# Optimization experiments

Measured on AMD Instinct MI355X. Metric: run time of the kernel, lower is better.

## Reference

```python
import jax, jax.numpy as jnp
import numpy as np

B, N, D, S, H, ITERS = 8, 2048, 256, 8, 256, 3
EPS = 1e-8
LN_EPS = 1e-5
SCALE = D ** -0.5


def _ln(x):
    # normalize over last axis (affine applied separately per slot)
    mu = jnp.mean(x, axis=-1, keepdims=True)
    var = jnp.var(x, axis=-1, keepdims=True)
    return (x - mu) / jnp.sqrt(var + LN_EPS)


def setup_inputs() -> dict:
    key = jax.random.key(0)
    ks = jax.random.split(key, 24)
    w = lambda k, shape, fan_in: jax.random.normal(k, shape, jnp.float32) / np.sqrt(fan_in)
    inp = {
        "inputs": jax.random.normal(ks[0], (B, N, D), jnp.float32),
        "slot_noise": jax.random.normal(ks[1], (B, S, D), jnp.float32),
        "slots_mu": jax.random.normal(ks[2], (1, S, D), jnp.float32),
        "slots_logsigma": 0.01 * jax.random.normal(ks[3], (1, S, D), jnp.float32),
        # per-slot LayerNorm affines [S, D]
        "g_in": jnp.ones((S, D), jnp.float32), "b_in": jnp.zeros((S, D), jnp.float32),
        "g_ns": jnp.ones((S, D), jnp.float32), "b_ns": jnp.zeros((S, D), jnp.float32),
        "g_pf": jnp.ones((S, D), jnp.float32), "b_pf": jnp.zeros((S, D), jnp.float32),
        # per-slot Linear weights [S, out, in] (torch convention)
        "Wq": w(ks[4], (S, D, D), D), "bq": jnp.zeros((S, D), jnp.float32),
        "Wk": w(ks[5], (S, D, D), D), "bk": jnp.zeros((S, D), jnp.float32),
        "Wv": w(ks[6], (S, D, D), D), "bv": jnp.zeros((S, D), jnp.float32),
        # per-slot GRUCell: [S, 3D, D] (gates order r, z, n as in torch)
        "W_ih": w(ks[7], (S, 3 * D, D), D), "b_ih": jnp.zeros((S, 3 * D), jnp.float32),
        "W_hh": w(ks[8], (S, 3 * D, D), D), "b_hh": jnp.zeros((S, 3 * D), jnp.float32),
        # per-slot MLP (dim -> hidden -> dim)
        "W1": w(ks[9], (S, H, D), D), "b1": jnp.zeros((S, H), jnp.float32),
        "W2": w(ks[10], (S, D, H), H), "b2": jnp.zeros((S, D), jnp.float32),
    }
    return inp


def slot_attention_fwd(inputs, slot_noise, slots_mu, slots_logsigma,
                       g_in, b_in, g_ns, b_ns, g_pf, b_pf,
                       Wq, bq, Wk, bk, Wv, bv,
                       W_ih, b_ih, W_hh, b_hh,
                       W1, b1, W2, b2):
    # slots init: mu + sigma * noise  -> [B, S, D]
    slots = slots_mu + jnp.exp(slots_logsigma) * slot_noise

    # per-slot LayerNorm of inputs: normalization is slot-independent, affine is per-slot
    xn = _ln(inputs)  # [B, N, D]
    inputs_n = xn[:, None, :, :] * g_in[None, :, None, :] + b_in[None, :, None, :]  # [B,S,N,D]

    # per-slot k/v projections as one batched GEMM over the slot axis
    k = jnp.einsum('bsnd,sod->bsno', inputs_n, Wk) + bk[None, :, None, :]  # [B,S,N,D]
    v = jnp.einsum('bsnd,sod->bsno', inputs_n, Wv) + bv[None, :, None, :]

    attn_ori = None
    for _ in range(ITERS):
        slots_prev = slots
        sn = _ln(slots) * g_ns[None] + b_ns[None]                     # [B,S,D]
        q = jnp.einsum('bsd,sod->bso', sn, Wq) + bq[None]             # [B,S,D]
        dots = jnp.einsum('bsd,bsnd->bsn', q, k) * SCALE              # [B,S,N]
        attn_ori = jax.nn.softmax(dots, axis=1) + EPS                 # softmax over slots
        attn = attn_ori / jnp.sum(attn_ori, axis=-1, keepdims=True)   # renormalize over n
        updates = jnp.einsum('bsnd,bsn->bsd', v, attn)                # [B,S,D]

        # per-slot GRUCell: h' = (1-z)*n + z*h
        gi = jnp.einsum('bsd,sod->bso', updates, W_ih) + b_ih[None]   # [B,S,3D]
        gh = jnp.einsum('bsd,sod->bso', slots_prev, W_hh) + b_hh[None]
        gi_r, gi_z, gi_n = jnp.split(gi, 3, axis=-1)
        gh_r, gh_z, gh_n = jnp.split(gh, 3, axis=-1)
        r = jax.nn.sigmoid(gi_r + gh_r)
        z = jax.nn.sigmoid(gi_z + gh_z)
        nn_ = jnp.tanh(gi_n + r * gh_n)
        slots = (1.0 - z) * nn_ + z * slots_prev

        # per-slot MLP residual
        pre = _ln(slots) * g_pf[None] + b_pf[None]
        h1 = jax.nn.relu(jnp.einsum('bsd,shd->bsh', pre, W1) + b1[None])
        slots = slots + jnp.einsum('bsh,sdh->bsd', h1, W2) + b2[None]

    return slots, attn_ori


def reference(inputs, slot_noise, slots_mu, slots_logsigma,
              g_in, b_in, g_ns, b_ns, g_pf, b_pf,
              Wq, bq, Wk, bk, Wv, bv,
              W_ih, b_ih, W_hh, b_hh,
              W1, b1, W2, b2):
    return slot_attention_fwd(inputs, slot_noise, slots_mu, slots_logsigma,
                              g_in, b_in, g_ns, b_ns, g_pf, b_pf,
                              Wq, bq, Wk, bk, Wv, bv,
                              W_ih, b_ih, W_hh, b_hh,
                              W1, b1, W2, b2)
```

## Files before the change

kernel.cpp:

```cpp
#include <hip/hip_runtime.h>
#include <hip/hip_bf16.h>


#define BB 8
#define NT 2048
#define DD 256
#define SS 8
#define HH 256

static constexpr float F_EPS   = 1e-8f;
static constexpr float F_LNEPS = 1e-5f;
static constexpr float F_SCALE = 0.0625f;

__device__ __forceinline__ float wredsum(float v) {
#pragma unroll
  for (int m = 32; m > 0; m >>= 1) v += __shfl_xor(v, m, 64);
  return v;
}
__device__ __forceinline__ float sigm(float x) { return 1.f / (1.f + __expf(-x)); }
__device__ __forceinline__ float tanhfast(float x) {
  float ax = fabsf(x);
  float e = __expf(2.f * ax);
  float t = 1.f - 2.f / (e + 1.f);
  return x < 0.f ? -t : t;
}

__global__ __launch_bounds__(256) void k_init(
    const float* __restrict__ Wk, const float* __restrict__ bk,
    const float* __restrict__ Wv, const float* __restrict__ bv,
    const float* __restrict__ b_in, const float* __restrict__ smu,
    const float* __restrict__ slsig, const float* __restrict__ noise,
    float* __restrict__ ck, float* __restrict__ cv, float* __restrict__ slots) {
  int blk = blockIdx.x;
  int t = threadIdx.x;
  if (blk < 32) {
    int s = blk >> 2, oq = blk & 3;
    int wid = t >> 6, lane = t & 63;
    float4 bi = ((const float4*)(b_in + s*DD))[lane];
    for (int r = 0; r < 16; ++r) {
      int o = oq*64 + wid*16 + r;
      float4 wk4 = ((const float4*)(Wk + ((size_t)s*DD + o)*DD))[lane];
      float4 wv4 = ((const float4*)(Wv + ((size_t)s*DD + o)*DD))[lane];
      float pk = wredsum(bi.x*wk4.x + bi.y*wk4.y + bi.z*wk4.z + bi.w*wk4.w);
      float pv = wredsum(bi.x*wv4.x + bi.y*wv4.y + bi.z*wv4.z + bi.w*wv4.w);
      if (lane == 0) {
        ck[s*DD+o] = pk + bk[s*DD+o];
        cv[s*DD+o] = pv + bv[s*DD+o];
      }
    }
  } else {
    int idx = (blk-32)*256 + t;
    int sd = idx & 2047;
    slots[idx] = smu[sd] + __expf(slsig[sd]) * noise[idx];
  }
}

__global__ __launch_bounds__(256) void k_init2(
    const float* __restrict__ Wq, const float* __restrict__ Wk,
    const float* __restrict__ bq, const float* __restrict__ ck,
    const float* __restrict__ g_in,
    float* __restrict__ Pg, float* __restrict__ vq,
    float* __restrict__ qcon, float* __restrict__ c0) {
  int blk = blockIdx.x;
  int t = threadIdx.x;
  if (blk < 512) {
    __shared__ float Ak[32*33], Aq[32*33];
    int s = blk >> 6, tile = blk & 63;
    int td = tile >> 3, te = tile & 7;
    int dl = t >> 5, el = t & 31;
    float acc[4] = {0.f,0.f,0.f,0.f};
    for (int o0 = 0; o0 < DD; o0 += 32) {
      __syncthreads();
      for (int i = t; i < 1024; i += 256) {
        int o = i >> 5, c = i & 31;
        Ak[o*33+c] = Wk[((size_t)s*DD + o0+o)*DD + td*32 + c];
        Aq[o*33+c] = Wq[((size_t)s*DD + o0+o)*DD + te*32 + c];
      }
      __syncthreads();
#pragma unroll 8
      for (int o = 0; o < 32; ++o) {
        float aq = Aq[o*33+el];
#pragma unroll
        for (int j = 0; j < 4; ++j)
          acc[j] += Ak[o*33 + dl*4 + j] * aq;
      }
    }
#pragma unroll
    for (int j = 0; j < 4; ++j) {
      int d = td*32 + dl*4 + j;
      Pg[((size_t)s*DD + d)*DD + te*32 + el] = g_in[s*DD + d] * acc[j];
    }
  } else {
    __shared__ float cvec[DD];
    __shared__ float part2[8*264];
    int idx = blk - 512;
    int s = idx >> 1, which = idx & 1;
    const float* W = which ? Wk : Wq;
    const float* vec = which ? bq : ck;
    cvec[t] = vec[s*DD + t];
    __syncthreads();
    int og = t >> 5, eg = t & 31;
    float acc[8] = {0.f,0.f,0.f,0.f,0.f,0.f,0.f,0.f};
    for (int oi = 0; oi < 32; ++oi) {
      int o = og*32 + oi;
      float cv2 = cvec[o];
      const float4* wrow = (const float4*)(W + ((size_t)s*DD + o)*DD + eg*8);
      float4 w0 = wrow[0], w1 = wrow[1];
      acc[0] += w0.x*cv2; acc[1] += w0.y*cv2; acc[2] += w0.z*cv2; acc[3] += w0.w*cv2;
      acc[4] += w1.x*cv2; acc[5] += w1.y*cv2; acc[6] += w1.z*cv2; acc[7] += w1.w*cv2;
    }
#pragma unroll
    for (int j = 0; j < 8; ++j) part2[og*264 + eg*8 + j] = acc[j];
    __syncthreads();
    float v = 0.f;
#pragma unroll
    for (int og2 = 0; og2 < 8; ++og2) v += part2[og2*264 + t];
    if (which) qcon[s*DD + t] = v * g_in[s*DD + t];
    else       vq[s*DD + t]   = v;
    if (which == 0 && t < 64) {
      float4 b4 = ((const float4*)(bq + s*DD))[t];
      float4 c4 = ((const float4*)(ck + s*DD))[t];
      float vv = wredsum(b4.x*c4.x + b4.y*c4.y + b4.z*c4.z + b4.w*c4.w);
      if (t == 0) c0[s] = vv;
    }
  }
}

__device__ __forceinline__ int x2i(int bb, int dd) { return bb*288 + (dd>>5)*36 + (dd&31); }

template <typename F>
__device__ __forceinline__ void gemv32(const float* __restrict__ Wrow0,
                                       const float* __restrict__ X2,
                                       float* __restrict__ part, F emit) {
  int t = threadIdx.x;
  int ol = t >> 3, dg = t & 7;
  const float4* wr = (const float4*)(Wrow0 + (size_t)ol*256 + (size_t)dg*32);
  __syncthreads();
  float acc[8] = {0.f,0.f,0.f,0.f,0.f,0.f,0.f,0.f};
#pragma unroll
  for (int j = 0; j < 8; ++j) {
    float4 w4 = wr[j];
    int xo = dg*36 + 4*j;
#pragma unroll
    for (int bbi = 0; bbi < 8; ++bbi) {
      float4 x4 = *(const float4*)&X2[bbi*288 + xo];
      acc[bbi] = fmaf(w4.x,x4.x, fmaf(w4.y,x4.y, fmaf(w4.z,x4.z, fmaf(w4.w,x4.w, acc[bbi]))));
    }
  }
#pragma unroll
  for (int bbi = 0; bbi < 8; ++bbi) part[(ol*8+bbi)*9 + dg] = acc[bbi];
  __syncthreads();
  int o = t >> 3, bbo = t & 7;
  const float* p = &part[(o*8+bbo)*9];
  float v = ((p[0]+p[1])+(p[2]+p[3]))+((p[4]+p[5])+(p[6]+p[7]));
  emit(o, bbo, v);
}

__global__ __launch_bounds__(256) void k_q2(
    const float* __restrict__ slots, const float* __restrict__ g_ns,
    const float* __restrict__ b_ns, const float* __restrict__ Pg,
    const float* __restrict__ qcon, const float* __restrict__ vq,
    const float* __restrict__ c0,
    float* __restrict__ qg, float* __restrict__ qc,
    float* __restrict__ axun, float* __restrict__ rsum) {
  __shared__ __align__(16) float X2[8*288];
  __shared__ float part[32*8*9];
  int blk = blockIdx.x;
  int s = blk >> 3, rc = blk & 7;
  int t = threadIdx.x;
  int wid = t >> 6, lane = t & 63;
  float4 g4 = ((const float4*)(g_ns + s*DD))[lane];
  float4 p4 = ((const float4*)(b_ns + s*DD))[lane];
#pragma unroll
  for (int half = 0; half < 2; ++half) {
    int bb2 = wid + half*4;
    const float4* src = (const float4*)(slots + (size_t)(bb2*8+s)*DD);
    float4 x = src[lane];
    float sv = wredsum(x.x+x.y+x.z+x.w);
    float sq = wredsum(x.x*x.x + x.y*x.y + x.z*x.z + x.w*x.w);
    float mu = sv*(1.f/DD), var = sq*(1.f/DD)-mu*mu, rs = rsqrtf(var+F_LNEPS);
    int base = bb2*288 + (lane>>3)*36 + (lane&7)*4;
    X2[base]   = (x.x-mu)*rs*g4.x + p4.x;
    X2[base+1] = (x.y-mu)*rs*g4.y + p4.y;
    X2[base+2] = (x.z-mu)*rs*g4.z + p4.z;
    X2[base+3] = (x.w-mu)*rs*g4.w + p4.w;
  }
  if (rc == 0) {
    for (int i = t; i < 2048; i += 256) {
      int bb2 = i >> 8, dd = i & 255;
      axun[(size_t)(bb2*8+s)*DD + dd] = 0.f;
    }
    if (t < 8) rsum[t*8+s] = 0.f;
  }
  __syncthreads();
  if (rc == 0) {
    int b = t >> 5, l32 = t & 31;
    float v = 0.f;
#pragma unroll
    for (int j = 0; j < 8; ++j)
      v += X2[b*288 + j*36 + l32] * vq[s*DD + j*32 + l32];
#pragma unroll
    for (int m = 16; m > 0; m >>= 1) v += __shfl_xor(v, m, 64);
    if (l32 == 0) qc[b*8+s] = v + c0[s];
  }
  gemv32(Pg + ((size_t)s*DD + rc*32)*DD, X2, part, [&](int o,int bb2,float v){
    qg[(size_t)(bb2*8+s)*DD + rc*32 + o] = v + qcon[s*DD + rc*32 + o];
  });
}

__global__ __launch_bounds__(256) void k_dots(
    const float* __restrict__ inputs, const float* __restrict__ qg,
    const float* __restrict__ qc, float* __restrict__ axun,
    float* __restrict__ rsum, float* __restrict__ attn_out, int write_attn) {
  __shared__ __align__(16) float qgl[SS*DD];
  __shared__ __align__(16) float xt[32*260];
  __shared__ float dl[8*33];
  __shared__ float qcl[8];
  __shared__ float rsl[8];
  int t = threadIdx.x;
  int b = blockIdx.x >> 5;
  int chunk = blockIdx.x & 31;
  int wid = t >> 6, lane = t & 63;
  for (int i = t; i < SS*DD; i += 256) qgl[i] = qg[(size_t)b*SS*DD + i];
  if (t < 8) { qcl[t] = qc[b*8+t]; rsl[t] = 0.f; }
  int si = t >> 5, ni = t & 31;
  float axa[8] = {0.f,0.f,0.f,0.f,0.f,0.f,0.f,0.f};
  for (int tile = 0; tile < 2; ++tile) {
    int n0 = (chunk*2 + tile) * 32;
    __syncthreads();
#pragma unroll
    for (int rr = 0; rr < 8; ++rr) {
      int r = wid*8 + rr;
      const float4* src = (const float4*)(inputs + ((size_t)b*NT + n0 + r)*DD);
      float4 x = src[lane];
      float sv = wredsum(x.x + x.y + x.z + x.w);
      float sq = wredsum(x.x*x.x + x.y*x.y + x.z*x.z + x.w*x.w);
      float mu = sv*(1.f/DD), var = sq*(1.f/DD)-mu*mu, rs = rsqrtf(var+F_LNEPS);
      float4 o;
      o.x=(x.x-mu)*rs; o.y=(x.y-mu)*rs; o.z=(x.z-mu)*rs; o.w=(x.w-mu)*rs;
      *(float4*)&xt[r*260 + lane*4] = o;
    }
    __syncthreads();
    float acc = 0.f;
    {
      const float4* xr = (const float4*)&xt[ni*260];
      const float4* qr = (const float4*)&qgl[si*DD];
#pragma unroll 8
      for (int j = 0; j < 64; ++j) {
        float4 a4 = xr[j]; float4 b4 = qr[j];
        acc += a4.x*b4.x + a4.y*b4.y + a4.z*b4.z + a4.w*b4.w;
      }
    }
    float dot = (acc + qcl[si]) * F_SCALE;
    dl[si*33+ni] = dot;
    __syncthreads();
    float m = dl[ni];
#pragma unroll
    for (int ss2 = 1; ss2 < 8; ++ss2) m = fmaxf(m, dl[ss2*33+ni]);
    float den = 0.f;
#pragma unroll
    for (int ss2 = 0; ss2 < 8; ++ss2) den += __expf(dl[ss2*33+ni] - m);
    float a = __expf(dot - m) / den + F_EPS;
    __syncthreads();
    dl[si*33+ni] = a;
    float rv = a;
#pragma unroll
    for (int mm = 16; mm > 0; mm >>= 1) rv += __shfl_xor(rv, mm, 64);
    if (ni == 0) rsl[si] += rv;
    if (write_attn) attn_out[(size_t)(b*8+si)*NT + n0 + ni] = a;
    __syncthreads();
#pragma unroll
    for (int n = 0; n < 32; ++n) {
      float x = xt[n*260 + t];
#pragma unroll
      for (int ss2 = 0; ss2 < 8; ++ss2) axa[ss2] += dl[ss2*33+n] * x;
    }
  }
#pragma unroll
  for (int ss2 = 0; ss2 < 8; ++ss2)
    atomicAdd(&axun[(size_t)(b*8+ss2)*DD + t], axa[ss2]);
  __syncthreads();
  if (t < 8) atomicAdd(&rsum[b*8+t], rsl[t]);
}

__global__ __launch_bounds__(256) void k_upd_gh(
    const float* __restrict__ axun, const float* __restrict__ rsum,
    const float* __restrict__ g_in, const float* __restrict__ Wv,
    const float* __restrict__ cv, const float* __restrict__ Whh,
    const float* __restrict__ bhh, const float* __restrict__ slots,
    float* __restrict__ upd, float* __restrict__ ghb) {
  __shared__ __align__(16) float X2[8*288];
  __shared__ float part[32*8*9];
  int blk = blockIdx.x;
  int s = blk >> 5, rc = blk & 31;
  int t = threadIdx.x;
  if (rc < 8) {
    for (int i = t; i < 2048; i += 256) {
      int bb2 = i >> 8, dd = i & 255;
      X2[x2i(bb2,dd)] = axun[(size_t)(bb2*8+s)*DD + dd] / rsum[bb2*8+s] * g_in[s*DD+dd];
    }
    int ob = rc*32;
    gemv32(Wv + ((size_t)s*DD + ob)*DD, X2, part, [&](int o,int bb2,float v){
      upd[(size_t)(bb2*8+s)*DD + ob + o] = v + cv[s*DD + ob + o];
    });
  } else {
    for (int i = t; i < 2048; i += 256) {
      int bb2 = i >> 8, dd = i & 255;
      X2[x2i(bb2,dd)] = slots[(size_t)(bb2*8+s)*DD + dd];
    }
    int ob = (rc-8)*32;
    gemv32(Whh + ((size_t)s*768 + ob)*DD, X2, part, [&](int o,int bb2,float v){
      ghb[(size_t)(bb2*8+s)*768 + ob + o] = v + bhh[s*768 + ob + o];
    });
  }
}

__global__ __launch_bounds__(256) void k_gru(
    const float* __restrict__ upd, const float* __restrict__ Wih,
    const float* __restrict__ bih, const float* __restrict__ ghb,
    const float* __restrict__ slots, float* __restrict__ smid) {
  __shared__ __align__(16) float X2[8*288];
  __shared__ float part[32*8*9];
  int blk = blockIdx.x;
  int s = blk >> 3, jc = blk & 7;
  int t = threadIdx.x;
  for (int i = t; i < 2048; i += 256) {
    int bb2 = i >> 8, dd = i & 255;
    X2[x2i(bb2,dd)] = upd[(size_t)(bb2*8+s)*DD + dd];
  }
  int jb = jc*32;
  float gir = 0.f, giz = 0.f, gin = 0.f;
  gemv32(Wih + ((size_t)s*768 + jb)*DD, X2, part,
         [&](int o,int bb2,float v){ (void)o; (void)bb2; gir = v + bih[s*768 + jb + (threadIdx.x>>3)]; });
  gemv32(Wih + ((size_t)s*768 + 256 + jb)*DD, X2, part,
         [&](int o,int bb2,float v){ (void)o; (void)bb2; giz = v + bih[s*768 + 256 + jb + (threadIdx.x>>3)]; });
  gemv32(Wih + ((size_t)s*768 + 512 + jb)*DD, X2, part,
         [&](int o,int bb2,float v){ (void)o; (void)bb2; gin = v + bih[s*768 + 512 + jb + (threadIdx.x>>3)]; });
  int j = t >> 3, bb2 = t & 7;
  size_t gb = (size_t)(bb2*8+s)*768 + jb + j;
  float r = sigm(gir + ghb[gb]);
  float z = sigm(giz + ghb[gb+256]);
  float nn2 = tanhfast(gin + r*ghb[gb+512]);
  size_t si2 = (size_t)(bb2*8+s)*DD + jb + j;
  float sp = slots[si2];
  smid[si2] = (1.f - z)*nn2 + z*sp;
}

__global__ __launch_bounds__(256) void k_mlp1(
    const float* __restrict__ smid, const float* __restrict__ g_pf,
    const float* __restrict__ b_pf, const float* __restrict__ W1,
    const float* __restrict__ b1, float* __restrict__ h1b) {
  __shared__ __align__(16) float X2[8*288];
  __shared__ float part[32*8*9];
  int blk = blockIdx.x;
  int s = blk >> 3, rc = blk & 7;
  int t = threadIdx.x;
  int wid = t >> 6, lane = t & 63;
#pragma unroll
  for (int half = 0; half < 2; ++half) {
    int bb2 = wid + half*4;
    const float4* src = (const float4*)(smid + (size_t)(bb2*8+s)*DD);
    float4 x = src[lane];
    float sv = wredsum(x.x+x.y+x.z+x.w);
    float sq = wredsum(x.x*x.x + x.y*x.y + x.z*x.z + x.w*x.w);
    float mu = sv*(1.f/DD), var = sq*(1.f/DD)-mu*mu, rs = rsqrtf(var+F_LNEPS);
    float4 g4 = ((const float4*)(g_pf + s*DD))[lane];
    float4 p4 = ((const float4*)(b_pf + s*DD))[lane];
    int base = bb2*288 + (lane>>3)*36 + (lane&7)*4;
    X2[base]   = (x.x-mu)*rs*g4.x + p4.x;
    X2[base+1] = (x.y-mu)*rs*g4.y + p4.y;
    X2[base+2] = (x.z-mu)*rs*g4.z + p4.z;
    X2[base+3] = (x.w-mu)*rs*g4.w + p4.w;
  }
  gemv32(W1 + ((size_t)s*HH + rc*32)*DD, X2, part, [&](int o,int bb2,float v){
    float rr = v + b1[s*HH + rc*32 + o];
    h1b[(size_t)(bb2*8+s)*HH + rc*32 + o] = fmaxf(rr, 0.f);
  });
}

__global__ __launch_bounds__(256) void k_mlp2(
    const float* __restrict__ h1b, const float* __restrict__ W2,
    const float* __restrict__ b2, const float* __restrict__ smid,
    float* __restrict__ slots, float* __restrict__ out_slots, int last) {
  __shared__ __align__(16) float X2[8*288];
  __shared__ float part[32*8*9];
  int blk = blockIdx.x;
  int s = blk >> 3, rc = blk & 7;
  int t = threadIdx.x;
  for (int i = t; i < 2048; i += 256) {
    int bb2 = i >> 8, dd = i & 255;
    X2[x2i(bb2,dd)] = h1b[(size_t)(bb2*8+s)*HH + dd];
  }
  gemv32(W2 + ((size_t)s*DD + rc*32)*HH, X2, part, [&](int o,int bb2,float v){
    int d = rc*32 + o;
    size_t idx = (size_t)(bb2*8+s)*DD + d;
    float rr = v + b2[s*DD + d] + smid[idx];
    slots[idx] = rr;
    if (last) out_slots[idx] = rr;
  });
}

extern "C" void kernel_launch(void* const* d_in, const int* in_sizes, int n_in,
                              void* d_out, int out_size, void* d_ws, size_t ws_size,
                              hipStream_t stream) {
  (void)in_sizes; (void)n_in; (void)out_size; (void)ws_size;
  const float* inputs = (const float*)d_in[0];
  const float* noise  = (const float*)d_in[1];
  const float* smu    = (const float*)d_in[2];
  const float* slsig  = (const float*)d_in[3];
  const float* g_in   = (const float*)d_in[4];
  const float* b_in   = (const float*)d_in[5];
  const float* g_ns   = (const float*)d_in[6];
  const float* b_ns   = (const float*)d_in[7];
  const float* g_pf   = (const float*)d_in[8];
  const float* b_pf   = (const float*)d_in[9];
  const float* Wq  = (const float*)d_in[10];
  const float* bq  = (const float*)d_in[11];
  const float* Wk  = (const float*)d_in[12];
  const float* bk  = (const float*)d_in[13];
  const float* Wv  = (const float*)d_in[14];
  const float* bv  = (const float*)d_in[15];
  const float* Wih = (const float*)d_in[16];
  const float* bih = (const float*)d_in[17];
  const float* Whh = (const float*)d_in[18];
  const float* bhh = (const float*)d_in[19];
  const float* W1  = (const float*)d_in[20];
  const float* b1  = (const float*)d_in[21];
  const float* W2  = (const float*)d_in[22];
  const float* b2  = (const float*)d_in[23];

  float* ws = (float*)d_ws;
  float* slots  = ws;
  float* smid   = slots + BB*SS*DD;
  float* ck     = smid + BB*SS*DD;
  float* cv     = ck + SS*DD;
  float* qg     = cv + SS*DD;
  float* qc     = qg + BB*SS*DD;
  float* rsum   = qc + BB*SS;
  float* axun   = rsum + BB*SS;
  float* upd    = axun + BB*SS*DD;
  float* ghb    = upd + BB*SS*DD;
  float* h1b    = ghb + (size_t)BB*SS*768;
  float* vq     = h1b + BB*SS*HH;
  float* qcon   = vq + SS*DD;
  float* c0     = qcon + SS*DD;
  float* Pg     = c0 + 64;

  float* out_slots = (float*)d_out;
  float* out_attn  = out_slots + BB*SS*DD;

  k_init<<<dim3(96), dim3(256), 0, stream>>>(Wk, bk, Wv, bv, b_in, smu, slsig, noise, ck, cv, slots);
  k_init2<<<dim3(528), dim3(256), 0, stream>>>(Wq, Wk, bq, ck, g_in, Pg, vq, qcon, c0);
  for (int it = 0; it < 3; ++it) {
    int last = (it == 2) ? 1 : 0;
    k_q2<<<dim3(64), dim3(256), 0, stream>>>(slots, g_ns, b_ns, Pg, qcon, vq, c0,
                                             qg, qc, axun, rsum);
    k_dots<<<dim3(256), dim3(256), 0, stream>>>(inputs, qg, qc, axun, rsum, out_attn, last);
    k_upd_gh<<<dim3(256), dim3(256), 0, stream>>>(axun, rsum, g_in, Wv, cv, Whh, bhh,
                                                  slots, upd, ghb);
    k_gru<<<dim3(64), dim3(256), 0, stream>>>(upd, Wih, bih, ghb, slots, smid);
    k_mlp1<<<dim3(64), dim3(256), 0, stream>>>(smid, g_pf, b_pf, W1, b1, h1b);
    k_mlp2<<<dim3(64), dim3(256), 0, stream>>>(h1b, W2, b2, smid, slots, out_slots, last);
  }
}
```

Measured before the change: 181.9 us.

## Fuse all per-iteration kernels into one persistent kernel with grid barriers

Replaces the two init kernels and the six per-iteration launches with a single persistent 256-block kernel. Phases are separated by a software grid barrier made of an atomic counter and spin-waiting, and the barrier counter is reset with a memset before launch. The Whh gate GEMV is moved to run alongside the query projection on otherwise idle blocks, so it no longer shares a phase with the update GEMV. This removes launch gaps but adds barrier latency, leaves most blocks idle in the 64-block phases, and depends on all 256 blocks being co-resident.

```diff
diff --git a/kernel.cpp b/kernel.cpp
--- a/kernel.cpp
+++ b/kernel.cpp
@@ -1,5 +1,4 @@
 #include <hip/hip_runtime.h>
-#include <hip/hip_bf16.h>
 
 
 #define BB 8
@@ -7,6 +6,7 @@
 #define DD 256
 #define SS 8
 #define HH 256
+#define GRID 256
 
 static constexpr float F_EPS   = 1e-8f;
 static constexpr float F_LNEPS = 1e-5f;
@@ -21,82 +21,125 @@
 __device__ __forceinline__ float tanhfast(float x) {
   float ax = fabsf(x);
   float e = __expf(2.f * ax);
-  float t = 1.f - 2.f / (e + 1.f);
-  return x < 0.f ? -t : t;
-}
-
-__global__ __launch_bounds__(256) void k_init(
-    const float* __restrict__ Wk, const float* __restrict__ bk,
-    const float* __restrict__ Wv, const float* __restrict__ bv,
-    const float* __restrict__ b_in, const float* __restrict__ smu,
-    const float* __restrict__ slsig, const float* __restrict__ noise,
-    float* __restrict__ ck, float* __restrict__ cv, float* __restrict__ slots) {
-  int blk = blockIdx.x;
+  float t2 = 1.f - 2.f / (e + 1.f);
+  return x < 0.f ? -t2 : t2;
+}
+__device__ __forceinline__ int x2i(int bb, int dd) { return bb*288 + (dd>>5)*36 + (dd&31); }
+
+__device__ __forceinline__ void gbar(int* bar, int target) {
+  __syncthreads();
+  if (threadIdx.x == 0) {
+    __threadfence();
+    __hip_atomic_fetch_add(bar, 1, __ATOMIC_RELAXED, __HIP_MEMORY_SCOPE_AGENT);
+    while (__hip_atomic_load(bar, __ATOMIC_RELAXED, __HIP_MEMORY_SCOPE_AGENT) < target)
+      __builtin_amdgcn_s_sleep(2);
+    __threadfence();
+  }
+  __syncthreads();
+}
+
+struct P {
+  const float *inputs,*noise,*smu,*slsig,*g_in,*b_in,*g_ns,*b_ns,*g_pf,*b_pf;
+  const float *Wq,*bq,*Wk,*bk,*Wv,*bv,*Wih,*bih,*Whh,*bhh,*W1,*b1,*W2,*b2;
+  float *slots,*smid,*ck,*cv,*qg,*qc,*rsum,*axun,*upd,*ghb,*h1b,*vq,*qcon,*c0,*Pg;
+  float *out_slots,*out_attn;
+  int *bar;
+};
+
+template <typename F>
+__device__ __forceinline__ void gemv32(const float* __restrict__ Wrow0,
+                                       const float* __restrict__ X2,
+                                       float* __restrict__ part, F emit) {
   int t = threadIdx.x;
+  int ol = t >> 3, dg = t & 7;
+  const float4* wr = (const float4*)(Wrow0 + (size_t)ol*256 + (size_t)dg*32);
+  __syncthreads();
+  float acc[8] = {0.f,0.f,0.f,0.f,0.f,0.f,0.f,0.f};
+#pragma unroll
+  for (int j = 0; j < 8; ++j) {
+    float4 w4 = wr[j];
+    int xo = dg*36 + 4*j;
+#pragma unroll
+    for (int bbi = 0; bbi < 8; ++bbi) {
+      float4 x4 = *(const float4*)&X2[bbi*288 + xo];
+      acc[bbi] = fmaf(w4.x,x4.x, fmaf(w4.y,x4.y, fmaf(w4.z,x4.z, fmaf(w4.w,x4.w, acc[bbi]))));
+    }
+  }
+#pragma unroll
+  for (int bbi = 0; bbi < 8; ++bbi) part[(ol*8+bbi)*9 + dg] = acc[bbi];
+  __syncthreads();
+  int o = t >> 3, bbo = t & 7;
+  const float* pp = &part[(o*8+bbo)*9];
+  float v = ((pp[0]+pp[1])+(pp[2]+pp[3]))+((pp[4]+pp[5])+(pp[6]+pp[7]));
+  emit(o, bbo, v);
+}
+
+__global__ __launch_bounds__(256, 1) void mega(P p) {
+  __shared__ __align__(16) float smem[10648];
+  const int blk = blockIdx.x;
+  const int t = threadIdx.x;
+  const int wid = t >> 6, lane = t & 63;
+  int* bar = p.bar;
+  int bc = 0;
+
   if (blk < 32) {
     int s = blk >> 2, oq = blk & 3;
-    int wid = t >> 6, lane = t & 63;
-    float4 bi = ((const float4*)(b_in + s*DD))[lane];
+    float4 bi = ((const float4*)(p.b_in + s*DD))[lane];
     for (int r = 0; r < 16; ++r) {
       int o = oq*64 + wid*16 + r;
-      float4 wk4 = ((const float4*)(Wk + ((size_t)s*DD + o)*DD))[lane];
-      float4 wv4 = ((const float4*)(Wv + ((size_t)s*DD + o)*DD))[lane];
+      float4 wk4 = ((const float4*)(p.Wk + ((size_t)s*DD + o)*DD))[lane];
+      float4 wv4 = ((const float4*)(p.Wv + ((size_t)s*DD + o)*DD))[lane];
       float pk = wredsum(bi.x*wk4.x + bi.y*wk4.y + bi.z*wk4.z + bi.w*wk4.w);
       float pv = wredsum(bi.x*wv4.x + bi.y*wv4.y + bi.z*wv4.z + bi.w*wv4.w);
       if (lane == 0) {
-        ck[s*DD+o] = pk + bk[s*DD+o];
-        cv[s*DD+o] = pv + bv[s*DD+o];
-      }
-    }
-  } else {
+        p.ck[s*DD+o] = pk + p.bk[s*DD+o];
+        p.cv[s*DD+o] = pv + p.bv[s*DD+o];
+      }
+    }
+  } else if (blk < 96) {
     int idx = (blk-32)*256 + t;
     int sd = idx & 2047;
-    slots[idx] = smu[sd] + __expf(slsig[sd]) * noise[idx];
-  }
-}
-
-__global__ __launch_bounds__(256) void k_init2(
-    const float* __restrict__ Wq, const float* __restrict__ Wk,
-    const float* __restrict__ bq, const float* __restrict__ ck,
-    const float* __restrict__ g_in,
-    float* __restrict__ Pg, float* __restrict__ vq,
-    float* __restrict__ qcon, float* __restrict__ c0) {
-  int blk = blockIdx.x;
-  int t = threadIdx.x;
-  if (blk < 512) {
-    __shared__ float Ak[32*33], Aq[32*33];
-    int s = blk >> 6, tile = blk & 63;
-    int td = tile >> 3, te = tile & 7;
-    int dl = t >> 5, el = t & 31;
-    float acc[4] = {0.f,0.f,0.f,0.f};
-    for (int o0 = 0; o0 < DD; o0 += 32) {
-      __syncthreads();
-      for (int i = t; i < 1024; i += 256) {
-        int o = i >> 5, c = i & 31;
-        Ak[o*33+c] = Wk[((size_t)s*DD + o0+o)*DD + td*32 + c];
-        Aq[o*33+c] = Wq[((size_t)s*DD + o0+o)*DD + te*32 + c];
-      }
-      __syncthreads();
+    p.slots[idx] = p.smu[sd] + __expf(p.slsig[sd]) * p.noise[idx];
+  }
+  {
+    float* Ak = smem;
+    float* Aq = smem + 1056;
+    for (int tile2 = blk; tile2 < 512; tile2 += 256) {
+      int s = tile2 >> 6, tile = tile2 & 63;
+      int td = tile >> 3, te = tile & 7;
+      int dli = t >> 5, el = t & 31;
+      float acc[4] = {0.f,0.f,0.f,0.f};
+      for (int o0 = 0; o0 < DD; o0 += 32) {
+        __syncthreads();
+        for (int i = t; i < 1024; i += 256) {
+          int o = i >> 5, c = i & 31;
+          Ak[o*33+c] = p.Wk[((size_t)s*DD + o0+o)*DD + td*32 + c];
+          Aq[o*33+c] = p.Wq[((size_t)s*DD + o0+o)*DD + te*32 + c];
+        }
+        __syncthreads();
 #pragma unroll 8
-      for (int o = 0; o < 32; ++o) {
-        float aq = Aq[o*33+el];
-#pragma unroll
-        for (int j = 0; j < 4; ++j)
-          acc[j] += Ak[o*33 + dl*4 + j] * aq;
-      }
-    }
-#pragma unroll
-    for (int j = 0; j < 4; ++j) {
-      int d = td*32 + dl*4 + j;
-      Pg[((size_t)s*DD + d)*DD + te*32 + el] = g_in[s*DD + d] * acc[j];
-    }
-  } else {
-    __shared__ float cvec[DD];
-    __shared__ float part2[8*264];
-    int idx = blk - 512;
-    int s = idx >> 1, which = idx & 1;
-    const float* W = which ? Wk : Wq;
-    const float* vec = which ? bq : ck;
+        for (int o = 0; o < 32; ++o) {
+          float aq = Aq[o*33+el];
+#pragma unroll
+          for (int j = 0; j < 4; ++j)
+            acc[j] += Ak[o*33 + dli*4 + j] * aq;
+        }
+      }
+#pragma unroll
+      for (int j = 0; j < 4; ++j) {
+        int d = td*32 + dli*4 + j;
+        p.Pg[((size_t)s*DD + d)*DD + te*32 + el] = p.g_in[s*DD + d] * acc[j];
+      }
+    }
+  }
+  gbar(bar, ++bc * GRID);
+
+  if (blk < 16) {
+    float* cvec  = smem;
+    float* part2 = smem + 256;
+    int s = blk >> 1, which = blk & 1;
+    const float* W = which ? p.Wk : p.Wq;
+    const float* vec = which ? p.bq : p.ck;
     cvec[t] = vec[s*DD + t];
     __syncthreads();
     int og = t >> 5, eg = t & 31;
@@ -115,351 +158,278 @@
     float v = 0.f;
 #pragma unroll
     for (int og2 = 0; og2 < 8; ++og2) v += part2[og2*264 + t];
-    if (which) qcon[s*DD + t] = v * g_in[s*DD + t];
-    else       vq[s*DD + t]   = v;
+    if (which) p.qcon[s*DD + t] = v * p.g_in[s*DD + t];
+    else       p.vq[s*DD + t]   = v;
     if (which == 0 && t < 64) {
-      float4 b4 = ((const float4*)(bq + s*DD))[t];
-      float4 c4 = ((const float4*)(ck + s*DD))[t];
+      float4 b4 = ((const float4*)(p.bq + s*DD))[t];
+      float4 c4 = ((const float4*)(p.ck + s*DD))[t];
       float vv = wredsum(b4.x*c4.x + b4.y*c4.y + b4.z*c4.z + b4.w*c4.w);
-      if (t == 0) c0[s] = vv;
-    }
-  }
-}
-
-__device__ __forceinline__ int x2i(int bb, int dd) { return bb*288 + (dd>>5)*36 + (dd&31); }
-
-template <typename F>
-__device__ __forceinline__ void gemv32(const float* __restrict__ Wrow0,
-                                       const float* __restrict__ X2,
-                                       float* __restrict__ part, F emit) {
-  int t = threadIdx.x;
-  int ol = t >> 3, dg = t & 7;
-  const float4* wr = (const float4*)(Wrow0 + (size_t)ol*256 + (size_t)dg*32);
-  __syncthreads();
-  float acc[8] = {0.f,0.f,0.f,0.f,0.f,0.f,0.f,0.f};
-#pragma unroll
-  for (int j = 0; j < 8; ++j) {
-    float4 w4 = wr[j];
-    int xo = dg*36 + 4*j;
-#pragma unroll
-    for (int bbi = 0; bbi < 8; ++bbi) {
-      float4 x4 = *(const float4*)&X2[bbi*288 + xo];
-      acc[bbi] = fmaf(w4.x,x4.x, fmaf(w4.y,x4.y, fmaf(w4.z,x4.z, fmaf(w4.w,x4.w, acc[bbi]))));
-    }
-  }
-#pragma unroll
-  for (int bbi = 0; bbi < 8; ++bbi) part[(ol*8+bbi)*9 + dg] = acc[bbi];
-  __syncthreads();
-  int o = t >> 3, bbo = t & 7;
-  const float* p = &part[(o*8+bbo)*9];
-  float v = ((p[0]+p[1])+(p[2]+p[3]))+((p[4]+p[5])+(p[6]+p[7]));
-  emit(o, bbo, v);
-}
-
-__global__ __launch_bounds__(256) void k_q2(
-    const float* __restrict__ slots, const float* __restrict__ g_ns,
-    const float* __restrict__ b_ns, const float* __restrict__ Pg,
-    const float* __restrict__ qcon, const float* __restrict__ vq,
-    const float* __restrict__ c0,
-    float* __restrict__ qg, float* __restrict__ qc,
-    float* __restrict__ axun, float* __restrict__ rsum) {
-  __shared__ __align__(16) float X2[8*288];
-  __shared__ float part[32*8*9];
-  int blk = blockIdx.x;
-  int s = blk >> 3, rc = blk & 7;
-  int t = threadIdx.x;
-  int wid = t >> 6, lane = t & 63;
-  float4 g4 = ((const float4*)(g_ns + s*DD))[lane];
-  float4 p4 = ((const float4*)(b_ns + s*DD))[lane];
-#pragma unroll
-  for (int half = 0; half < 2; ++half) {
-    int bb2 = wid + half*4;
-    const float4* src = (const float4*)(slots + (size_t)(bb2*8+s)*DD);
-    float4 x = src[lane];
-    float sv = wredsum(x.x+x.y+x.z+x.w);
-    float sq = wredsum(x.x*x.x + x.y*x.y + x.z*x.z + x.w*x.w);
-    float mu = sv*(1.f/DD), var = sq*(1.f/DD)-mu*mu, rs = rsqrtf(var+F_LNEPS);
-    int base = bb2*288 + (lane>>3)*36 + (lane&7)*4;
-    X2[base]   = (x.x-mu)*rs*g4.x + p4.x;
-    X2[base+1] = (x.y-mu)*rs*g4.y + p4.y;
-    X2[base+2] = (x.z-mu)*rs*g4.z + p4.z;
-    X2[base+3] = (x.w-mu)*rs*g4.w + p4.w;
-  }
-  if (rc == 0) {
-    for (int i = t; i < 2048; i += 256) {
-      int bb2 = i >> 8, dd = i & 255;
-      axun[(size_t)(bb2*8+s)*DD + dd] = 0.f;
-    }
-    if (t < 8) rsum[t*8+s] = 0.f;
-  }
-  __syncthreads();
-  if (rc == 0) {
-    int b = t >> 5, l32 = t & 31;
-    float v = 0.f;
-#pragma unroll
-    for (int j = 0; j < 8; ++j)
-      v += X2[b*288 + j*36 + l32] * vq[s*DD + j*32 + l32];
-#pragma unroll
-    for (int m = 16; m > 0; m >>= 1) v += __shfl_xor(v, m, 64);
-    if (l32 == 0) qc[b*8+s] = v + c0[s];
-  }
-  gemv32(Pg + ((size_t)s*DD + rc*32)*DD, X2, part, [&](int o,int bb2,float v){
-    qg[(size_t)(bb2*8+s)*DD + rc*32 + o] = v + qcon[s*DD + rc*32 + o];
-  });
-}
-
-__global__ __launch_bounds__(256) void k_dots(
-    const float* __restrict__ inputs, const float* __restrict__ qg,
-    const float* __restrict__ qc, float* __restrict__ axun,
-    float* __restrict__ rsum, float* __restrict__ attn_out, int write_attn) {
-  __shared__ __align__(16) float qgl[SS*DD];
-  __shared__ __align__(16) float xt[32*260];
-  __shared__ float dl[8*33];
-  __shared__ float qcl[8];
-  __shared__ float rsl[8];
-  int t = threadIdx.x;
-  int b = blockIdx.x >> 5;
-  int chunk = blockIdx.x & 31;
-  int wid = t >> 6, lane = t & 63;
-  for (int i = t; i < SS*DD; i += 256) qgl[i] = qg[(size_t)b*SS*DD + i];
-  if (t < 8) { qcl[t] = qc[b*8+t]; rsl[t] = 0.f; }
-  int si = t >> 5, ni = t & 31;
-  float axa[8] = {0.f,0.f,0.f,0.f,0.f,0.f,0.f,0.f};
-  for (int tile = 0; tile < 2; ++tile) {
-    int n0 = (chunk*2 + tile) * 32;
-    __syncthreads();
-#pragma unroll
-    for (int rr = 0; rr < 8; ++rr) {
-      int r = wid*8 + rr;
-      const float4* src = (const float4*)(inputs + ((size_t)b*NT + n0 + r)*DD);
-      float4 x = src[lane];
-      float sv = wredsum(x.x + x.y + x.z + x.w);
-      float sq = wredsum(x.x*x.x + x.y*x.y + x.z*x.z + x.w*x.w);
-      float mu = sv*(1.f/DD), var = sq*(1.f/DD)-mu*mu, rs = rsqrtf(var+F_LNEPS);
-      float4 o;
-      o.x=(x.x-mu)*rs; o.y=(x.y-mu)*rs; o.z=(x.z-mu)*rs; o.w=(x.w-mu)*rs;
-      *(float4*)&xt[r*260 + lane*4] = o;
-    }
-    __syncthreads();
-    float acc = 0.f;
+      if (t == 0) p.c0[s] = vv;
+    }
+  }
+  gbar(bar, ++bc * GRID);
+
+  for (int it = 0; it < 3; ++it) {
+    const int last = (it == 2);
+    float* X2   = smem;
+    float* part = smem + 2304;
+
+    if (blk < 64) {
+      int s = blk >> 3, rc = blk & 7;
+      float4 g4 = ((const float4*)(p.g_ns + s*DD))[lane];
+      float4 p4 = ((const float4*)(p.b_ns + s*DD))[lane];
+#pragma unroll
+      for (int half = 0; half < 2; ++half) {
+        int bb2 = wid + half*4;
+        const float4* src = (const float4*)(p.slots + (size_t)(bb2*8+s)*DD);
+        float4 x = src[lane];
+        float sv = wredsum(x.x+x.y+x.z+x.w);
+        float sq = wredsum(x.x*x.x + x.y*x.y + x.z*x.z + x.w*x.w);
+        float mu = sv*(1.f/DD), var = sq*(1.f/DD)-mu*mu, rs = rsqrtf(var+F_LNEPS);
+        int base = bb2*288 + (lane>>3)*36 + (lane&7)*4;
+        X2[base]   = (x.x-mu)*rs*g4.x + p4.x;
+        X2[base+1] = (x.y-mu)*rs*g4.y + p4.y;
+        X2[base+2] = (x.z-mu)*rs*g4.z + p4.z;
+        X2[base+3] = (x.w-mu)*rs*g4.w + p4.w;
+      }
+      if (rc == 0) {
+        for (int i = t; i < 2048; i += 256) {
+          int bb2 = i >> 8, dd = i & 255;
+          p.axun[(size_t)(bb2*8+s)*DD + dd] = 0.f;
+        }
+        if (t < 8) p.rsum[t*8+s] = 0.f;
+      }
+      __syncthreads();
+      if (rc == 0) {
+        int b = t >> 5, l32 = t & 31;
+        float v = 0.f;
+#pragma unroll
+        for (int j = 0; j < 8; ++j)
+          v += X2[b*288 + j*36 + l32] * p.vq[s*DD + j*32 + l32];
+#pragma unroll
+        for (int m = 16; m > 0; m >>= 1) v += __shfl_xor(v, m, 64);
+        if (l32 == 0) p.qc[b*8+s] = v + p.c0[s];
+      }
+      gemv32(p.Pg + ((size_t)s*DD + rc*32)*DD, X2, part, [&](int o,int bb2,float v){
+        p.qg[(size_t)(bb2*8+s)*DD + rc*32 + o] = v + p.qcon[s*DD + rc*32 + o];
+      });
+    } else {
+      int idx = blk - 64;
+      int s = idx / 24, jt = idx % 24;
+      for (int i = t; i < 2048; i += 256) {
+        int bb2 = i >> 8, dd = i & 255;
+        X2[x2i(bb2,dd)] = p.slots[(size_t)(bb2*8+s)*DD + dd];
+      }
+      int ob = jt*32;
+      gemv32(p.Whh + ((size_t)s*768 + ob)*DD, X2, part, [&](int o,int bb2,float v){
+        p.ghb[(size_t)(bb2*8+s)*768 + ob + o] = v + p.bhh[s*768 + ob + o];
+      });
+    }
+    gbar(bar, ++bc * GRID);
+
     {
-      const float4* xr = (const float4*)&xt[ni*260];
-      const float4* qr = (const float4*)&qgl[si*DD];
+      float* qgl = smem;
+      float* xt  = smem + 2048;
+      float* dl  = smem + 10368;
+      float* qcl = smem + 10632;
+      float* rsl = smem + 10640;
+      int b = blk >> 5;
+      int chunk = blk & 31;
+      for (int i = t; i < SS*DD; i += 256) qgl[i] = p.qg[(size_t)b*SS*DD + i];
+      if (t < 8) { qcl[t] = p.qc[b*8+t]; rsl[t] = 0.f; }
+      int si = t >> 5, ni = t & 31;
+      float axa[8] = {0.f,0.f,0.f,0.f,0.f,0.f,0.f,0.f};
+      for (int tile = 0; tile < 2; ++tile) {
+        int n0 = (chunk*2 + tile) * 32;
+        __syncthreads();
+#pragma unroll
+        for (int rr = 0; rr < 8; ++rr) {
+          int r = wid*8 + rr;
+          const float4* src = (const float4*)(p.inputs + ((size_t)b*NT + n0 + r)*DD);
+          float4 x = src[lane];
+          float sv = wredsum(x.x + x.y + x.z + x.w);
+          float sq = wredsum(x.x*x.x + x.y*x.y + x.z*x.z + x.w*x.w);
+          float mu = sv*(1.f/DD), var = sq*(1.f/DD)-mu*mu, rs = rsqrtf(var+F_LNEPS);
+          float4 o;
+          o.x=(x.x-mu)*rs; o.y=(x.y-mu)*rs; o.z=(x.z-mu)*rs; o.w=(x.w-mu)*rs;
+          *(float4*)&xt[r*260 + lane*4] = o;
+        }
+        __syncthreads();
+        float acc = 0.f;
+        {
+          const float4* xr = (const float4*)&xt[ni*260];
+          const float4* qr = (const float4*)&qgl[si*DD];
 #pragma unroll 8
-      for (int j = 0; j < 64; ++j) {
-        float4 a4 = xr[j]; float4 b4 = qr[j];
-        acc += a4.x*b4.x + a4.y*b4.y + a4.z*b4.z + a4.w*b4.w;
-      }
-    }
-    float dot = (acc + qcl[si]) * F_SCALE;
-    dl[si*33+ni] = dot;
-    __syncthreads();
-    float m = dl[ni];
-#pragma unroll
-    for (int ss2 = 1; ss2 < 8; ++ss2) m = fmaxf(m, dl[ss2*33+ni]);
-    float den = 0.f;
-#pragma unroll
-    for (int ss2 = 0; ss2 < 8; ++ss2) den += __expf(dl[ss2*33+ni] - m);
-    float a = __expf(dot - m) / den + F_EPS;
-    __syncthreads();
-    dl[si*33+ni] = a;
-    float rv = a;
-#pragma unroll
-    for (int mm = 16; mm > 0; mm >>= 1) rv += __shfl_xor(rv, mm, 64);
-    if (ni == 0) rsl[si] += rv;
-    if (write_attn) attn_out[(size_t)(b*8+si)*NT + n0 + ni] = a;
-    __syncthreads();
-#pragma unroll
-    for (int n = 0; n < 32; ++n) {
-      float x = xt[n*260 + t];
-#pragma unroll
-      for (int ss2 = 0; ss2 < 8; ++ss2) axa[ss2] += dl[ss2*33+n] * x;
-    }
-  }
-#pragma unroll
-  for (int ss2 = 0; ss2 < 8; ++ss2)
-    atomicAdd(&axun[(size_t)(b*8+ss2)*DD + t], axa[ss2]);
-  __syncthreads();
-  if (t < 8) atomicAdd(&rsum[b*8+t], rsl[t]);
-}
-
-__global__ __launch_bounds__(256) void k_upd_gh(
-    const float* __restrict__ axun, const float* __restrict__ rsum,
-    const float* __restrict__ g_in, const float* __restrict__ Wv,
-    const float* __restrict__ cv, const float* __restrict__ Whh,
-    const float* __restrict__ bhh, const float* __restrict__ slots,
-    float* __restrict__ upd, float* __restrict__ ghb) {
-  __shared__ __align__(16) float X2[8*288];
-  __shared__ float part[32*8*9];
-  int blk = blockIdx.x;
-  int s = blk >> 5, rc = blk & 31;
-  int t = threadIdx.x;
-  if (rc < 8) {
-    for (int i = t; i < 2048; i += 256) {
-      int bb2 = i >> 8, dd = i & 255;
-      X2[x2i(bb2,dd)] = axun[(size_t)(bb2*8+s)*DD + dd] / rsum[bb2*8+s] * g_in[s*DD+dd];
-    }
-    int ob = rc*32;
-    gemv32(Wv + ((size_t)s*DD + ob)*DD, X2, part, [&](int o,int bb2,float v){
-      upd[(size_t)(bb2*8+s)*DD + ob + o] = v + cv[s*DD + ob + o];
-    });
-  } else {
-    for (int i = t; i < 2048; i += 256) {
-      int bb2 = i >> 8, dd = i & 255;
-      X2[x2i(bb2,dd)] = slots[(size_t)(bb2*8+s)*DD + dd];
-    }
-    int ob = (rc-8)*32;
-    gemv32(Whh + ((size_t)s*768 + ob)*DD, X2, part, [&](int o,int bb2,float v){
-      ghb[(size_t)(bb2*8+s)*768 + ob + o] = v + bhh[s*768 + ob + o];
-    });
-  }
-}
-
-__global__ __launch_bounds__(256) void k_gru(
-    const float* __restrict__ upd, const float* __restrict__ Wih,
-    const float* __restrict__ bih, const float* __restrict__ ghb,
-    const float* __restrict__ slots, float* __restrict__ smid) {
-  __shared__ __align__(16) float X2[8*288];
-  __shared__ float part[32*8*9];
-  int blk = blockIdx.x;
-  int s = blk >> 3, jc = blk & 7;
-  int t = threadIdx.x;
-  for (int i = t; i < 2048; i += 256) {
-    int bb2 = i >> 8, dd = i & 255;
-    X2[x2i(bb2,dd)] = upd[(size_t)(bb2*8+s)*DD + dd];
-  }
-  int jb = jc*32;
-  float gir = 0.f, giz = 0.f, gin = 0.f;
-  gemv32(Wih + ((size_t)s*768 + jb)*DD, X2, part,
-         [&](int o,int bb2,float v){ (void)o; (void)bb2; gir = v + bih[s*768 + jb + (threadIdx.x>>3)]; });
-  gemv32(Wih + ((size_t)s*768 + 256 + jb)*DD, X2, part,
-         [&](int o,int bb2,float v){ (void)o; (void)bb2; giz = v + bih[s*768 + 256 + jb + (threadIdx.x>>3)]; });
-  gemv32(Wih + ((size_t)s*768 + 512 + jb)*DD, X2, part,
-         [&](int o,int bb2,float v){ (void)o; (void)bb2; gin = v + bih[s*768 + 512 + jb + (threadIdx.x>>3)]; });
-  int j = t >> 3, bb2 = t & 7;
-  size_t gb = (size_t)(bb2*8+s)*768 + jb + j;
-  float r = sigm(gir + ghb[gb]);
-  float z = sigm(giz + ghb[gb+256]);
-  float nn2 = tanhfast(gin + r*ghb[gb+512]);
-  size_t si2 = (size_t)(bb2*8+s)*DD + jb + j;
-  float sp = slots[si2];
-  smid[si2] = (1.f - z)*nn2 + z*sp;
-}
-
-__global__ __launch_bounds__(256) void k_mlp1(
-    const float* __restrict__ smid, const float* __restrict__ g_pf,
-    const float* __restrict__ b_pf, const float* __restrict__ W1,
-    const float* __restrict__ b1, float* __restrict__ h1b) {
-  __shared__ __align__(16) float X2[8*288];
-  __shared__ float part[32*8*9];
-  int blk = blockIdx.x;
-  int s = blk >> 3, rc = blk & 7;
-  int t = threadIdx.x;
-  int wid = t >> 6, lane = t & 63;
-#pragma unroll
-  for (int half = 0; half < 2; ++half) {
-    int bb2 = wid + half*4;
-    const float4* src = (const float4*)(smid + (size_t)(bb2*8+s)*DD);
-    float4 x = src[lane];
-    float sv = wredsum(x.x+x.y+x.z+x.w);
-    float sq = wredsum(x.x*x.x + x.y*x.y + x.z*x.z + x.w*x.w);
-    float mu = sv*(1.f/DD), var = sq*(1.f/DD)-mu*mu, rs = rsqrtf(var+F_LNEPS);
-    float4 g4 = ((const float4*)(g_pf + s*DD))[lane];
-    float4 p4 = ((const float4*)(b_pf + s*DD))[lane];
-    int base = bb2*288 + (lane>>3)*36 + (lane&7)*4;
-    X2[base]   = (x.x-mu)*rs*g4.x + p4.x;
-    X2[base+1] = (x.y-mu)*rs*g4.y + p4.y;
-    X2[base+2] = (x.z-mu)*rs*g4.z + p4.z;
-    X2[base+3] = (x.w-mu)*rs*g4.w + p4.w;
-  }
-  gemv32(W1 + ((size_t)s*HH + rc*32)*DD, X2, part, [&](int o,int bb2,float v){
-    float rr = v + b1[s*HH + rc*32 + o];
-    h1b[(size_t)(bb2*8+s)*HH + rc*32 + o] = fmaxf(rr, 0.f);
-  });
-}
-
-__global__ __launch_bounds__(256) void k_mlp2(
-    const float* __restrict__ h1b, const float* __restrict__ W2,
-    const float* __restrict__ b2, const float* __restrict__ smid,
-    float* __restrict__ slots, float* __restrict__ out_slots, int last) {
-  __shared__ __align__(16) float X2[8*288];
-  __shared__ float part[32*8*9];
-  int blk = blockIdx.x;
-  int s = blk >> 3, rc = blk & 7;
-  int t = threadIdx.x;
-  for (int i = t; i < 2048; i += 256) {
-    int bb2 = i >> 8, dd = i & 255;
-    X2[x2i(bb2,dd)] = h1b[(size_t)(bb2*8+s)*HH + dd];
-  }
-  gemv32(W2 + ((size_t)s*DD + rc*32)*HH, X2, part, [&](int o,int bb2,float v){
-    int d = rc*32 + o;
-    size_t idx = (size_t)(bb2*8+s)*DD + d;
-    float rr = v + b2[s*DD + d] + smid[idx];
-    slots[idx] = rr;
-    if (last) out_slots[idx] = rr;
-  });
+          for (int j = 0; j < 64; ++j) {
+            float4 a4 = xr[j]; float4 b4 = qr[j];
+            acc += a4.x*b4.x + a4.y*b4.y + a4.z*b4.z + a4.w*b4.w;
+          }
+        }
+        float dot = (acc + qcl[si]) * F_SCALE;
+        dl[si*33+ni] = dot;
+        __syncthreads();
+        float m = dl[ni];
+#pragma unroll
+        for (int ss2 = 1; ss2 < 8; ++ss2) m = fmaxf(m, dl[ss2*33+ni]);
+        float den = 0.f;
+#pragma unroll
+        for (int ss2 = 0; ss2 < 8; ++ss2) den += __expf(dl[ss2*33+ni] - m);
+        float a = __expf(dot - m) / den + F_EPS;
+        __syncthreads();
+        dl[si*33+ni] = a;
+        float rv = a;
+#pragma unroll
+        for (int mm = 16; mm > 0; mm >>= 1) rv += __shfl_xor(rv, mm, 64);
+        if (ni == 0) rsl[si] += rv;
+        if (last) p.out_attn[(size_t)(b*8+si)*NT + n0 + ni] = a;
+        __syncthreads();
+#pragma unroll
+        for (int n = 0; n < 32; ++n) {
+          float x = xt[n*260 + t];
+#pragma unroll
+          for (int ss2 = 0; ss2 < 8; ++ss2) axa[ss2] += dl[ss2*33+n] * x;
+        }
+      }
+#pragma unroll
+      for (int ss2 = 0; ss2 < 8; ++ss2)
+        atomicAdd(&p.axun[(size_t)(b*8+ss2)*DD + t], axa[ss2]);
+      __syncthreads();
+      if (t < 8) atomicAdd(&p.rsum[b*8+t], rsl[t]);
+    }
+    gbar(bar, ++bc * GRID);
+
+    if (blk < 64) {
+      int s = blk >> 3, rc = blk & 7;
+      for (int i = t; i < 2048; i += 256) {
+        int bb2 = i >> 8, dd = i & 255;
+        X2[x2i(bb2,dd)] = p.axun[(size_t)(bb2*8+s)*DD + dd] / p.rsum[bb2*8+s] * p.g_in[s*DD+dd];
+      }
+      int ob = rc*32;
+      gemv32(p.Wv + ((size_t)s*DD + ob)*DD, X2, part, [&](int o,int bb2,float v){
+        p.upd[(size_t)(bb2*8+s)*DD + ob + o] = v + p.cv[s*DD + ob + o];
+      });
+    }
+    gbar(bar, ++bc * GRID);
+
+    if (blk < 64) {
+      int s = blk >> 3, jc = blk & 7;
+      for (int i = t; i < 2048; i += 256) {
+        int bb2 = i >> 8, dd = i & 255;
+        X2[x2i(bb2,dd)] = p.upd[(size_t)(bb2*8+s)*DD + dd];
+      }
+      int jb = jc*32;
+      float gir = 0.f, giz = 0.f, gin = 0.f;
+      gemv32(p.Wih + ((size_t)s*768 + jb)*DD, X2, part,
+             [&](int o,int bb2,float v){ (void)o; (void)bb2; gir = v + p.bih[s*768 + jb + (threadIdx.x>>3)]; });
+      gemv32(p.Wih + ((size_t)s*768 + 256 + jb)*DD, X2, part,
+             [&](int o,int bb2,float v){ (void)o; (void)bb2; giz = v + p.bih[s*768 + 256 + jb + (threadIdx.x>>3)]; });
+      gemv32(p.Wih + ((size_t)s*768 + 512 + jb)*DD, X2, part,
+             [&](int o,int bb2,float v){ (void)o; (void)bb2; gin = v + p.bih[s*768 + 512 + jb + (threadIdx.x>>3)]; });
+      int j = t >> 3, bb2 = t & 7;
+      size_t gb = (size_t)(bb2*8+s)*768 + jb + j;
+      float r = sigm(gir + p.ghb[gb]);
+      float z = sigm(giz + p.ghb[gb+256]);
+      float nn2 = tanhfast(gin + r*p.ghb[gb+512]);
+      size_t si2 = (size_t)(bb2*8+s)*DD + jb + j;
+      float sp = p.slots[si2];
+      p.smid[si2] = (1.f - z)*nn2 + z*sp;
+    }
+    gbar(bar, ++bc * GRID);
+
+    if (blk < 64) {
+      int s = blk >> 3, rc = blk & 7;
+#pragma unroll
+      for (int half = 0; half < 2; ++half) {
+        int bb2 = wid + half*4;
+        const float4* src = (const float4*)(p.smid + (size_t)(bb2*8+s)*DD);
+        float4 x = src[lane];
+        float sv = wredsum(x.x+x.y+x.z+x.w);
+        float sq = wredsum(x.x*x.x + x.y*x.y + x.z*x.z + x.w*x.w);
+        float mu = sv*(1.f/DD), var = sq*(1.f/DD)-mu*mu, rs = rsqrtf(var+F_LNEPS);
+        float4 g4 = ((const float4*)(p.g_pf + s*DD))[lane];
+        float4 p4 = ((const float4*)(p.b_pf + s*DD))[lane];
+        int base = bb2*288 + (lane>>3)*36 + (lane&7)*4;
+        X2[base]   = (x.x-mu)*rs*g4.x + p4.x;
+        X2[base+1] = (x.y-mu)*rs*g4.y + p4.y;
+        X2[base+2] = (x.z-mu)*rs*g4.z + p4.z;
+        X2[base+3] = (x.w-mu)*rs*g4.w + p4.w;
+      }
+      gemv32(p.W1 + ((size_t)s*HH + rc*32)*DD, X2, part, [&](int o,int bb2,float v){
+        float rr = v + p.b1[s*HH + rc*32 + o];
+        p.h1b[(size_t)(bb2*8+s)*HH + rc*32 + o] = fmaxf(rr, 0.f);
+      });
+    }
+    gbar(bar, ++bc * GRID);
+
+    if (blk < 64) {
+      int s = blk >> 3, rc = blk & 7;
+      for (int i = t; i < 2048; i += 256) {
+        int bb2 = i >> 8, dd = i & 255;
+        X2[x2i(bb2,dd)] = p.h1b[(size_t)(bb2*8+s)*HH + dd];
+      }
+      gemv32(p.W2 + ((size_t)s*DD + rc*32)*HH, X2, part, [&](int o,int bb2,float v){
+        int d = rc*32 + o;
+        size_t idx = (size_t)(bb2*8+s)*DD + d;
+        float rr = v + p.b2[s*DD + d] + p.smid[idx];
+        p.slots[idx] = rr;
+        if (last) p.out_slots[idx] = rr;
+      });
+    }
+    if (it != 2) gbar(bar, ++bc * GRID);
+  }
 }
 
 extern "C" void kernel_launch(void* const* d_in, const int* in_sizes, int n_in,
                               void* d_out, int out_size, void* d_ws, size_t ws_size,
                               hipStream_t stream) {
   (void)in_sizes; (void)n_in; (void)out_size; (void)ws_size;
-  const float* inputs = (const float*)d_in[0];
-  const float* noise  = (const float*)d_in[1];
-  const float* smu    = (const float*)d_in[2];
-  const float* slsig  = (const float*)d_in[3];
-  const float* g_in   = (const float*)d_in[4];
-  const float* b_in   = (const float*)d_in[5];
-  const float* g_ns   = (const float*)d_in[6];
-  const float* b_ns   = (const float*)d_in[7];
-  const float* g_pf   = (const float*)d_in[8];
-  const float* b_pf   = (const float*)d_in[9];
-  const float* Wq  = (const float*)d_in[10];
-  const float* bq  = (const float*)d_in[11];
-  const float* Wk  = (const float*)d_in[12];
-  const float* bk  = (const float*)d_in[13];
-  const float* Wv  = (const float*)d_in[14];
-  const float* bv  = (const float*)d_in[15];
-  const float* Wih = (const float*)d_in[16];
-  const float* bih = (const float*)d_in[17];
-  const float* Whh = (const float*)d_in[18];
-  const float* bhh = (const float*)d_in[19];
-  const float* W1  = (const float*)d_in[20];
-  const float* b1  = (const float*)d_in[21];
-  const float* W2  = (const float*)d_in[22];
-  const float* b2  = (const float*)d_in[23];
-
   float* ws = (float*)d_ws;
-  float* slots  = ws;
-  float* smid   = slots + BB*SS*DD;
-  float* ck     = smid + BB*SS*DD;
-  float* cv     = ck + SS*DD;
-  float* qg     = cv + SS*DD;
-  float* qc     = qg + BB*SS*DD;
-  float* rsum   = qc + BB*SS;
-  float* axun   = rsum + BB*SS;
-  float* upd    = axun + BB*SS*DD;
-  float* ghb    = upd + BB*SS*DD;
-  float* h1b    = ghb + (size_t)BB*SS*768;
-  float* vq     = h1b + BB*SS*HH;
-  float* qcon   = vq + SS*DD;
-  float* c0     = qcon + SS*DD;
-  float* Pg     = c0 + 64;
-
-  float* out_slots = (float*)d_out;
-  float* out_attn  = out_slots + BB*SS*DD;
-
-  k_init<<<dim3(96), dim3(256), 0, stream>>>(Wk, bk, Wv, bv, b_in, smu, slsig, noise, ck, cv, slots);
-  k_init2<<<dim3(528), dim3(256), 0, stream>>>(Wq, Wk, bq, ck, g_in, Pg, vq, qcon, c0);
-  for (int it = 0; it < 3; ++it) {
-    int last = (it == 2) ? 1 : 0;
-    k_q2<<<dim3(64), dim3(256), 0, stream>>>(slots, g_ns, b_ns, Pg, qcon, vq, c0,
-                                             qg, qc, axun, rsum);
-    k_dots<<<dim3(256), dim3(256), 0, stream>>>(inputs, qg, qc, axun, rsum, out_attn, last);
-    k_upd_gh<<<dim3(256), dim3(256), 0, stream>>>(axun, rsum, g_in, Wv, cv, Whh, bhh,
-                                                  slots, upd, ghb);
-    k_gru<<<dim3(64), dim3(256), 0, stream>>>(upd, Wih, bih, ghb, slots, smid);
-    k_mlp1<<<dim3(64), dim3(256), 0, stream>>>(smid, g_pf, b_pf, W1, b1, h1b);
-    k_mlp2<<<dim3(64), dim3(256), 0, stream>>>(h1b, W2, b2, smid, slots, out_slots, last);
-  }
-}
+  P p;
+  p.inputs = (const float*)d_in[0];
+  p.noise  = (const float*)d_in[1];
+  p.smu    = (const float*)d_in[2];
+  p.slsig  = (const float*)d_in[3];
+  p.g_in   = (const float*)d_in[4];
+  p.b_in   = (const float*)d_in[5];
+  p.g_ns   = (const float*)d_in[6];
+  p.b_ns   = (const float*)d_in[7];
+  p.g_pf   = (const float*)d_in[8];
+  p.b_pf   = (const float*)d_in[9];
+  p.Wq  = (const float*)d_in[10];
+  p.bq  = (const float*)d_in[11];
+  p.Wk  = (const float*)d_in[12];
+  p.bk  = (const float*)d_in[13];
+  p.Wv  = (const float*)d_in[14];
+  p.bv  = (const float*)d_in[15];
+  p.Wih = (const float*)d_in[16];
+  p.bih = (const float*)d_in[17];
+  p.Whh = (const float*)d_in[18];
+  p.bhh = (const float*)d_in[19];
+  p.W1  = (const float*)d_in[20];
+  p.b1  = (const float*)d_in[21];
+  p.W2  = (const float*)d_in[22];
+  p.b2  = (const float*)d_in[23];
+
+  p.slots = ws;                         ws += BB*SS*DD;
+  p.smid  = ws;                         ws += BB*SS*DD;
+  p.ck    = ws;                         ws += SS*DD;
+  p.cv    = ws;                         ws += SS*DD;
+  p.qg    = ws;                         ws += BB*SS*DD;
+  p.qc    = ws;                         ws += BB*SS;
+  p.rsum  = ws;                         ws += BB*SS;
+  p.axun  = ws;                         ws += BB*SS*DD;
+  p.upd   = ws;                         ws += BB*SS*DD;
+  p.ghb   = ws;                         ws += BB*SS*768;
+  p.h1b   = ws;                         ws += BB*SS*HH;
+  p.vq    = ws;                         ws += SS*DD;
+  p.qcon  = ws;                         ws += SS*DD;
+  p.c0    = ws;                         ws += 64;
+  p.Pg    = ws;                         ws += SS*DD*DD;
+  p.bar   = (int*)ws;
+
+  p.out_slots = (float*)d_out;
+  p.out_attn  = p.out_slots + BB*SS*DD;
+
+  hipMemsetAsync((void*)p.bar, 0, 64, stream);
+  mega<<<dim3(GRID), dim3(256), 0, stream>>>(p);
+}
```

New measurement: 528.6 us. 191% more time.
